# Kernel optimization log

Measured on AMD Instinct MI355X. Metric: run time of the kernel, lower is better.

Reference implementation:

```python
import jax, jax.numpy as jnp
import numpy as np

BN_EPS = 1e-5


def fps(xyz, npoint):
    # farthest point sampling; xyz: (B,N,3) -> (B,npoint) int32, starts at index 0 (torch convention)
    B, N, _ = xyz.shape
    def step(carry, _):
        dist, last = carry
        lp = jnp.take_along_axis(xyz, last[:, None, None], axis=1)  # (B,1,3)
        d = jnp.sum((xyz - lp) ** 2, -1)                             # (B,N)
        dist = jnp.minimum(dist, d)
        nxt = jnp.argmax(dist, -1).astype(jnp.int32)
        return (dist, nxt), nxt
    init = (jnp.full((B, N), 1e10, xyz.dtype), jnp.zeros((B,), jnp.int32))
    _, rest = jax.lax.scan(step, init, None, length=npoint - 1)
    return jnp.concatenate([jnp.zeros((1, B), jnp.int32), rest], 0).T  # (B,npoint)


def knn_idx(xyz, centers, k):
    # xyz (B,N,3), centers (B,S,3) -> (B,S,k) nearest-neighbor indices
    d = (jnp.sum(centers ** 2, -1)[:, :, None]
         + jnp.sum(xyz ** 2, -1)[:, None, :]
         - 2.0 * jnp.einsum('bsc,bnc->bsn', centers, xyz))
    _, idx = jax.lax.top_k(-d, k)
    return idx


def group(feat, idx):
    # feat (B,N,C), idx (B,S,K) -> (B,S,K,C)
    return jax.vmap(lambda f, i: f[i])(feat, idx)


def sa_knn(xyz, points, npoint, nsample, w1, b1, w2, b2):
    # xyz (B,N,3), points (B,N,C); returns new_xyz (B,S,3), new_points (B,S,Cout)
    fidx = fps(xyz, npoint)
    new_xyz = jnp.take_along_axis(xyz, fidx[:, :, None], axis=1)        # (B,S,3)
    idx = knn_idx(xyz, new_xyz, nsample)                                 # (B,S,K)
    g_xyz = group(xyz, idx) - new_xyz[:, :, None, :]                     # relative coords
    g_pts = group(points, idx)
    x = jnp.concatenate([g_xyz, g_pts], -1)                              # (B,S,K,3+C)
    x = jax.nn.relu(jnp.einsum('bskc,oc->bsko', x, w1) + b1)
    x = jnp.einsum('bskc,oc->bsko', x, w2) + b2                          # last conv: no activation
    return new_xyz, jnp.max(x, 2)                                        # max over neighbors


def sa_all(xyz, points, w1, b1, w2, b2):
    # group_all: concat xyz+points over all N, shared MLP, max over N -> (B,Cout)
    x = jnp.concatenate([xyz, points], -1)                               # (B,N,3+C)
    x = jax.nn.relu(jnp.einsum('bnc,oc->bno', x, w1) + b1)
    x = jnp.einsum('bnc,oc->bno', x, w2) + b2
    return jnp.max(x, 1)


def fc_head(x, w1, b1, g1, be1, w2, b2, g2, be2):
    # Linear + BN(eval, running mean=0/var=1) + ReLU, twice; Dropout = identity in eval
    s = 1.0 / np.sqrt(1.0 + BN_EPS)
    x = jax.nn.relu(g1 * ((x @ w1.T + b1) * s) + be1)
    x = jax.nn.relu(g2 * ((x @ w2.T + b2) * s) + be2)
    return x


def forward(point_cloud, sa1_w1, sa1_b1, sa1_w2, sa1_b2,
            sa2_w1, sa2_b1, sa2_w2, sa2_b2,
            sa3_w1, sa3_b1, sa3_w2, sa3_b2,
            fc_w1, fc_b1, fc_g1, fc_be1, fc_w2, fc_b2, fc_g2, fc_be2):
    xyz = jnp.transpose(point_cloud, (0, 2, 1))  # (B,N,3)
    nsamples2 = (16, 32, 48)
    logits, codes = [], []
    for i in range(3):  # three structurally distinct branches
        x1, p1 = sa_knn(xyz, xyz, 512, 16, sa1_w1[i], sa1_b1[i], sa1_w2[i], sa1_b2[i])
        x2, p2 = sa_knn(x1, p1, 128, nsamples2[i], sa2_w1[i], sa2_b1[i], sa2_w2[i], sa2_b2[i])
        code = sa_all(x2, p2, sa3_w1[i], sa3_b1[i], sa3_w2[i], sa3_b2[i])   # (B,512)
        logits.append(fc_head(code, fc_w1[i], fc_b1[i], fc_g1[i], fc_be1[i],
                              fc_w2[i], fc_b2[i], fc_g2[i], fc_be2[i]))      # (B,128)
        codes.append(code)
    return tuple(logits) + tuple(codes)


def setup_inputs():
    key = jax.random.key(0)
    ks = iter(jax.random.split(key, 16))
    def w(shape, s=0.05):
        return jax.random.normal(next(ks), shape, jnp.float32) * s
    B, N = 32, 2048
    inp = {'point_cloud': jax.random.normal(next(ks), (B, 3, N), jnp.float32)}
    inp.update(
        sa1_w1=w((3, 64, 6)), sa1_b1=jnp.zeros((3, 64)), sa1_w2=w((3, 128, 64)), sa1_b2=jnp.zeros((3, 128)),
        sa2_w1=w((3, 128, 131)), sa2_b1=jnp.zeros((3, 128)), sa2_w2=w((3, 256, 128)), sa2_b2=jnp.zeros((3, 256)),
        sa3_w1=w((3, 512, 259)), sa3_b1=jnp.zeros((3, 512)), sa3_w2=w((3, 512, 512)), sa3_b2=jnp.zeros((3, 512)),
        fc_w1=w((3, 256, 512)), fc_b1=jnp.zeros((3, 256)), fc_g1=jnp.ones((3, 256)), fc_be1=jnp.zeros((3, 256)),
        fc_w2=w((3, 128, 256)), fc_b2=jnp.zeros((3, 128)), fc_g2=jnp.ones((3, 128)), fc_be2=jnp.zeros((3, 128)),
    )
    return inp


def reference(point_cloud, sa1_w1, sa1_b1, sa1_w2, sa1_b2,
              sa2_w1, sa2_b1, sa2_w2, sa2_b2,
              sa3_w1, sa3_b1, sa3_w2, sa3_b2,
              fc_w1, fc_b1, fc_g1, fc_be1, fc_w2, fc_b2, fc_g2, fc_be2):
    return forward(point_cloud, sa1_w1, sa1_b1, sa1_w2, sa1_b2,
                   sa2_w1, sa2_b1, sa2_w2, sa2_b2,
                   sa3_w1, sa3_b1, sa3_w2, sa3_b2,
                   fc_w1, fc_b1, fc_g1, fc_be1, fc_w2, fc_b2, fc_g2, fc_be2)
```

## Files before the change

### kernel.cpp

```cpp
#include <hip/hip_runtime.h>
#include <hip/hip_bf16.h>
#include <math.h>

#define DEVI __device__ __forceinline__

static constexpr int BB = 32, NN = 2048, S1 = 512, S2 = 128;

typedef float f32x4 __attribute__((ext_vector_type(4)));
typedef short s16x8 __attribute__((ext_vector_type(8)));

static constexpr size_t OFF_XS   = 0;
static constexpr size_t OFF_YS   = OFF_XS + (size_t)BB*NN;
static constexpr size_t OFF_ZS   = OFF_YS + (size_t)BB*NN;
static constexpr size_t OFF_SSQ  = OFF_ZS + (size_t)BB*NN;
static constexpr size_t OFF_NX1X = OFF_SSQ + (size_t)BB*NN;
static constexpr size_t OFF_NX1Y = OFF_NX1X + (size_t)BB*S1;
static constexpr size_t OFF_NX1Z = OFF_NX1Y + (size_t)BB*S1;
static constexpr size_t OFF_NX2X = OFF_NX1Z + (size_t)BB*S1;
static constexpr size_t OFF_NX2Y = OFF_NX2X + (size_t)BB*S2;
static constexpr size_t OFF_NX2Z = OFF_NX2Y + (size_t)BB*S2;
static constexpr size_t OFF_CODE = OFF_NX2Z + (size_t)BB*S2;
static constexpr size_t OFF_O3P  = OFF_CODE + (size_t)3*BB*512;
static constexpr size_t OFF_P1   = OFF_O3P + (size_t)3*BB*4*512;
static constexpr size_t OFF_X3   = OFF_P1 + (size_t)3*BB*S1*128;
static constexpr size_t OFF_H3   = OFF_X3 + (size_t)3*BB*S2*260;
static constexpr size_t OFF_W    = OFF_H3 + (size_t)3*BB*S2*512;
static constexpr size_t W1A  = OFF_W;
static constexpr size_t B1A  = W1A + 3*64*6;
static constexpr size_t W2A  = B1A + 3*64;
static constexpr size_t B2A  = W2A + 3*128*64;
static constexpr size_t W1B  = B2A + 3*128;
static constexpr size_t B1B  = W1B + 3*128*132;
static constexpr size_t W2B  = B1B + 3*128;
static constexpr size_t B2B  = W2B + 3*256*128;
static constexpr size_t W1C  = B2B + 3*256;
static constexpr size_t B1C  = W1C + 3*512*260;
static constexpr size_t W2C  = B1C + 3*512;
static constexpr size_t B2C  = W2C + 3*512*512;
static constexpr size_t FW1  = B2C + 3*512;
static constexpr size_t FB1  = FW1 + 3*256*512;
static constexpr size_t FG1  = FB1 + 3*256;
static constexpr size_t FBE1 = FG1 + 3*256;
static constexpr size_t FW2  = FBE1 + 3*256;
static constexpr size_t FB2  = FW2 + 3*128*256;
static constexpr size_t FG2  = FB2 + 3*128;
static constexpr size_t FBE2 = FG2 + 3*128;
static constexpr size_t OFF_KNN1 = FBE2 + 3*128;
static constexpr size_t OFF_KNN2 = OFF_KNN1 + (size_t)BB*S1*16;
static constexpr size_t OFF_W1BF = OFF_KNN2 + (size_t)BB*S2*48;
static constexpr size_t OFF_W2BF = OFF_W1BF + 30720;
static constexpr size_t OFF_W1CBH = OFF_W2BF + 49152;
static constexpr size_t OFF_W1CBL = OFF_W1CBH + 221184;
static constexpr size_t OFF_W2CBH = OFF_W1CBL + 221184;
static constexpr size_t OFF_W2CBL = OFF_W2CBH + 393216;
static constexpr size_t OFF_X3BH  = OFF_W2CBL + 393216;
static constexpr size_t OFF_X3BL  = OFF_X3BH + 1769472;
static constexpr size_t OFF_H3BH  = OFF_X3BL + 1769472;
static constexpr size_t OFF_H3BL  = OFF_H3BH + 3145728;
static constexpr size_t OFF_W2ABH = OFF_H3BL + 3145728;
static constexpr size_t OFF_W2ABL = OFF_W2ABH + 12288;
static constexpr size_t WS_FLOATS = OFF_W2ABL + 12288;

__device__ __align__(16) float g_ws[WS_FLOATS];
__device__ int g_is_f32;
__device__ int g_flip;
__device__ int g_bad;
__device__ int g_nz;

DEVI float bf2f(const __hip_bfloat16 v){ return __bfloat162float(v); }
DEVI float rn_add(float a, float b){ return __fadd_rn(a,b); }
DEVI float rn_mul(float a, float b){ return __fmul_rn(a,b); }
DEVI float rn_sub(float a, float b){ return __fsub_rn(a,b); }
DEVI float sq3(float x,float y,float z){ return rn_add(rn_add(rn_mul(x,x),rn_mul(y,y)),rn_mul(z,z)); }

DEVI float ldany(const void* s, size_t i, int isf){
  return isf ? ((const float*)s)[i] : bf2f(((const __hip_bfloat16*)s)[i]);
}
DEVI unsigned short f2bf(float f){
  unsigned u = __float_as_uint(f);
  unsigned r = (u + 0x7FFFu + ((u>>16)&1u)) >> 16;
  return (unsigned short)r;
}
DEVI float bfbits2f(unsigned short h){ return __uint_as_float(((unsigned)h)<<16); }
DEVI void mfma16(f32x4& d, s16x8 a, s16x8 b){
  asm volatile("v_mfma_f32_16x16x32_bf16 %0, %1, %2, %0" : "+v"(d) : "v"(a), "v"(b));
}
DEVI void mfma_guard(f32x4& d){
  asm volatile("s_nop 7\n\ts_nop 7\n\ts_nop 2" : "+v"(d));
}

#define DPPF(dst, src, CTRL) dst = __uint_as_float((unsigned)__builtin_amdgcn_update_dpp(\
    (int)__float_as_uint(src), (int)__float_as_uint(src), CTRL, 0xF, 0xF, false))
#define DPPI(dst, src, CTRL) dst = __builtin_amdgcn_update_dpp(src, src, CTRL, 0xF, 0xF, false)
#define RED_STEP(CTRL) { float ov; int oi; DPPF(ov, best, CTRL); DPPI(oi, bidx, CTRL); \
  if (ov > best || (ov == best && oi < bidx)){ best = ov; bidx = oi; } }
#define WAVE_ARGMAX() RED_STEP(0xB1) RED_STEP(0x4E) RED_STEP(0x124) RED_STEP(0x128) RED_STEP(0x142) RED_STEP(0x143)

#define REDMIN_STEP(CTRL) { float ov; int oi; DPPF(ov, best, CTRL); DPPI(oi, bidx, CTRL); \
  if (ov < best || (ov == best && oi < bidx)){ best = ov; bidx = oi; } }
#define WAVE_ARGMIN() REDMIN_STEP(0xB1) REDMIN_STEP(0x4E) REDMIN_STEP(0x124) REDMIN_STEP(0x128) REDMIN_STEP(0x142) REDMIN_STEP(0x143)

__global__ __launch_bounds__(256) void init_detect_kernel(const void* __restrict__ pc){
  __shared__ int s_cnt[256];
  int t = threadIdx.x;
  if (t==0){ g_flip=0; g_bad=0; g_nz=0; }
  const unsigned short* h = (const unsigned short*)pc;
  int weird = 0;
  for (int i=t; i<4096; i+=256){
    unsigned short v = h[2*i];
    int e = (v >> 7) & 0xFF;
    if (e == 0xFF || e < 90 || e > 140) weird++;
  }
  s_cnt[t] = weird; __syncthreads();
  for (int o=128;o>0;o>>=1){ if (t<o) s_cnt[t]+=s_cnt[t+o]; __syncthreads(); }
  if (t==0) g_is_f32 = (s_cnt[0] > 1024) ? 1 : 0;
}

struct ParamPtrs { const void* p[20]; };

DEVI void cvt_arr(const void* s, float* d, int n, int g, int gs, int isf){
  for (int i=g;i<n;i+=gs) d[i] = ldany(s,i,isf);
}
DEVI void cvt_pad(const void* s, float* d, int rows, int cin, int cinp, int g, int gs, int isf){
  int tot = rows*cinp;
  for (int i=g;i<tot;i+=gs){ int r=i/cinp, c=i%cinp; d[i] = (c<cin)? ldany(s,(size_t)r*cin+c,isf) : 0.f; }
}

__global__ __launch_bounds__(256) void cvtprep_kernel(ParamPtrs pp, const void* __restrict__ pc, int mode){
  if (mode==1 && g_flip==0) return;
  const int isf = g_is_f32 ^ mode;
  if (blockIdx.x < 256){
    int i = blockIdx.x*256 + threadIdx.x;
    int b = i >> 11, n = i & 2047;
    float x = ldany(pc, (size_t)(b*3+0)*2048 + n, isf);
    float y = ldany(pc, (size_t)(b*3+1)*2048 + n, isf);
    float z = ldany(pc, (size_t)(b*3+2)*2048 + n, isf);
    g_ws[OFF_XS+i]=x; g_ws[OFF_YS+i]=y; g_ws[OFF_ZS+i]=z;
    g_ws[OFF_SSQ+i]=sq3(x,y,z);
    return;
  }
  int g = (blockIdx.x-256)*256 + threadIdx.x; int gs = 512*256;
  float* ws = g_ws;
  cvt_arr(pp.p[0],  ws+W1A, 3*64*6, g, gs, isf);
  cvt_arr(pp.p[1],  ws+B1A, 3*64, g, gs, isf);
  cvt_arr(pp.p[2],  ws+W2A, 3*128*64, g, gs, isf);
  cvt_arr(pp.p[3],  ws+B2A, 3*128, g, gs, isf);
  cvt_pad(pp.p[4],  ws+W1B, 3*128, 131, 132, g, gs, isf);
  cvt_arr(pp.p[5],  ws+B1B, 3*128, g, gs, isf);
  cvt_arr(pp.p[6],  ws+W2B, 3*256*128, g, gs, isf);
  cvt_arr(pp.p[7],  ws+B2B, 3*256, g, gs, isf);
  cvt_pad(pp.p[8],  ws+W1C, 3*512, 259, 260, g, gs, isf);
  cvt_arr(pp.p[9],  ws+B1C, 3*512, g, gs, isf);
  cvt_arr(pp.p[10], ws+W2C, 3*512*512, g, gs, isf);
  cvt_arr(pp.p[11], ws+B2C, 3*512, g, gs, isf);
  cvt_arr(pp.p[12], ws+FW1, 3*256*512, g, gs, isf);
  cvt_arr(pp.p[13], ws+FB1, 3*256, g, gs, isf);
  cvt_arr(pp.p[14], ws+FG1, 3*256, g, gs, isf);
  cvt_arr(pp.p[15], ws+FBE1,3*256, g, gs, isf);
  cvt_arr(pp.p[16], ws+FW2, 3*128*256, g, gs, isf);
  cvt_arr(pp.p[17], ws+FB2, 3*128, g, gs, isf);
  cvt_arr(pp.p[18], ws+FG2, 3*128, g, gs, isf);
  cvt_arr(pp.p[19], ws+FBE2,3*128, g, gs, isf);
}

__global__ __launch_bounds__(256) void scan_check_kernel(){
  size_t off; int n, g, gs;
  if (blockIdx.x < 128){ off = OFF_XS; n = 3*BB*NN; g = blockIdx.x*256 + threadIdx.x; gs = 128*256; }
  else { off = FW1; n = 3*256*512; g = (blockIdx.x-128)*256 + threadIdx.x; gs = 128*256; }
  int bad=0, nz=0;
  for (int i=g;i<n;i+=gs){
    float v = g_ws[off + i];
    if (v != v || fabsf(v) > 1e4f) bad=1;
    if (fabsf(v) > 1e-20f) nz=1;
  }
  unsigned long long mb = __ballot(bad), mn = __ballot(nz);
  if ((threadIdx.x & 63)==0){
    if (mb) atomicOr(&g_bad, 1);
    if (mn) atomicOr(&g_nz, 1);
  }
}

__global__ __launch_bounds__(64) void resolve_flip_kernel(){
  if (threadIdx.x==0){
    g_flip = (g_bad || !g_nz) ? 1 : 0;
    g_bad = 0; g_nz = 0;
  }
}

DEVI void cvt_bf16_body(int g, int gs){
  unsigned short* w1d = (unsigned short*)(g_ws + OFF_W1BF);
  for (int i=g; i<3*128*160; i+=gs){
    int br = i/(128*160); int rem = i%(128*160); int h = rem/160; int c = rem%160;
    float v = (c<132) ? g_ws[W1B + ((size_t)br*128 + h)*132 + c] : 0.f;
    w1d[i] = f2bf(v);
  }
  unsigned short* w2d = (unsigned short*)(g_ws + OFF_W2BF);
  for (int i=g; i<3*256*128; i+=gs) w2d[i] = f2bf(g_ws[W2B + i]);
  unsigned short* w1ch = (unsigned short*)(g_ws + OFF_W1CBH);
  unsigned short* w1cl = (unsigned short*)(g_ws + OFF_W1CBL);
  for (int i=g; i<3*512*288; i+=gs){
    int br = i/(512*288); int rem = i%(512*288); int n = rem/288; int c = rem%288;
    float v = (c<260) ? g_ws[W1C + ((size_t)br*512 + n)*260 + c] : 0.f;
    unsigned short hi = f2bf(v);
    w1ch[i] = hi; w1cl[i] = f2bf(v - bfbits2f(hi));
  }
  unsigned short* w2ch = (unsigned short*)(g_ws + OFF_W2CBH);
  unsigned short* w2cl = (unsigned short*)(g_ws + OFF_W2CBL);
  for (int i=g; i<3*512*512; i+=gs){
    float v = g_ws[W2C + i];
    unsigned short hi = f2bf(v);
    w2ch[i] = hi; w2cl[i] = f2bf(v - bfbits2f(hi));
  }
  unsigned short* w2ah = (unsigned short*)(g_ws + OFF_W2ABH);
  unsigned short* w2al = (unsigned short*)(g_ws + OFF_W2ABL);
  for (int i=g; i<3*128*64; i+=gs){
    float v = g_ws[W2A + i];
    unsigned short hi = f2bf(v);
    w2ah[i] = hi; w2al[i] = f2bf(v - bfbits2f(hi));
  }
}

static constexpr int SP1 = 171, SP2 = 342;

#define FPS_DECL(J) float px##J, py##J, pz##J, dd##J;
#define FPS_LD256A(J) { int n=(J)*256+t; px##J=xs[n]; py##J=ys[n]; pz##J=zs[n]; dd##J=1e10f; xl[n]=px##J; yl[n]=py##J; zl[n]=pz##J; }
#define FPS_LD256B(J) { int n=(J)*256+t; px##J=xs[n]; py##J=ys[n]; pz##J=zs[n]; dd##J=ddg[n]; xl[n]=px##J; yl[n]=py##J; zl[n]=pz##J; }
#define FPS_SAVE(J) ddg[(J)*256+t]=dd##J;
#define FPS_LD64(J) { int n=(J)*64+t; px##J=xs[n]; py##J=ys[n]; pz##J=zs[n]; dd##J=1e10f; xl[n]=px##J; yl[n]=py##J; zl[n]=pz##J; }
#define FPS_UPD(J) { float dx=rn_sub(px##J,lx), dy=rn_sub(py##J,ly), dz=rn_sub(pz##J,lz); float d=sq3(dx,dy,dz); dd##J=fminf(dd##J,d); }
#define FPS_T1(J,JA,JB) float v##J; int q##J; { bool c = dd##JB > dd##JA; v##J = c? dd##JB : dd##JA; q##J = c? (JB) : (JA); }
#define FPS_T2(JA,JB) { bool c = v##JB > v##JA; v##JA = c? v##JB : v##JA; q##JA = c? q##JB : q##JA; }

#define FPS1_ITER_BODY() \
    FPS_UPD(0) FPS_UPD(1) FPS_UPD(2) FPS_UPD(3) FPS_UPD(4) FPS_UPD(5) FPS_UPD(6) FPS_UPD(7) \
    FPS_T1(0,0,1) FPS_T1(1,2,3) FPS_T1(2,4,5) FPS_T1(3,6,7) \
    FPS_T2(0,1) FPS_T2(2,3) \
    FPS_T2(0,2) \
    float best = v0; int bidx = q0*256 + t; \
    WAVE_ARGMAX() \
    int par = i & 1; \
    if ((t&63)==63){ s_val[par][wave]=best; s_idx[par][wave]=bidx; } \
    __syncthreads(); \
    float va = s_val[par][0], vb = s_val[par][1], vc = s_val[par][2], vd = s_val[par][3]; \
    int ia = s_idx[par][0], ib = s_idx[par][1], ic = s_idx[par][2], id_ = s_idx[par][3]; \
    if (vb > va || (vb == va && ib < ia)){ va = vb; ia = ib; } \
    if (vd > vc || (vd == vc && id_ < ic)){ vc = vd; ic = id_; } \
    if (vc > va || (vc == va && ic < ia)){ va = vc; ia = ic; } \
    int gidx = ia; \
    lx = xl[gidx]; ly = yl[gidx]; lz = zl[gidx]; \
    if (t==0){ nx[i]=lx; ny[i]=ly; nz[i]=lz; }

#define FPS1_BLOCK_SETUP() \
  const int b = blockIdx.x; \
  const int wave = t >> 6; \
  const float* xs = g_ws + OFF_XS + (size_t)b*NN; \
  const float* ys = g_ws + OFF_YS + (size_t)b*NN; \
  const float* zs = g_ws + OFF_ZS + (size_t)b*NN; \
  float* nx = g_ws + OFF_NX1X + (size_t)b*S1; \
  float* ny = g_ws + OFF_NX1Y + (size_t)b*S1; \
  float* nz = g_ws + OFF_NX1Z + (size_t)b*S1; \
  float* ddg = g_ws + OFF_X3 + (size_t)b*NN; \
  __shared__ float xl[NN], yl[NN], zl[NN]; \
  __shared__ float s_val[2][4]; __shared__ int s_idx[2][4]; \
  FPS_DECL(0) FPS_DECL(1) FPS_DECL(2) FPS_DECL(3) FPS_DECL(4) FPS_DECL(5) FPS_DECL(6) FPS_DECL(7)

#define FPS1_BLOCK_SETUP_U(SM) \
  const int b = blockIdx.x; \
  const int wave = t >> 6; \
  const float* xs = g_ws + OFF_XS + (size_t)b*NN; \
  const float* ys = g_ws + OFF_YS + (size_t)b*NN; \
  const float* zs = g_ws + OFF_ZS + (size_t)b*NN; \
  float* nx = g_ws + OFF_NX1X + (size_t)b*S1; \
  float* ny = g_ws + OFF_NX1Y + (size_t)b*S1; \
  float* nz = g_ws + OFF_NX1Z + (size_t)b*S1; \
  float* ddg = g_ws + OFF_X3 + (size_t)b*NN; \
  float* xl = (float*)(SM); float* yl = xl + NN; float* zl = yl + NN; \
  float (*s_val)[4] = (float(*)[4])(zl + NN); \
  int (*s_idx)[4] = (int(*)[4])((char*)(zl + NN) + 32); \
  FPS_DECL(0) FPS_DECL(1) FPS_DECL(2) FPS_DECL(3) FPS_DECL(4) FPS_DECL(5) FPS_DECL(6) FPS_DECL(7)

__global__ __launch_bounds__(256,1) void fps1A_cvt_kernel(){
  const int t = threadIdx.x;
  if (blockIdx.x >= 32){
    cvt_bf16_body((blockIdx.x-32)*256 + t, 256*256);
    return;
  }
  FPS1_BLOCK_SETUP()
  FPS_LD256A(0) FPS_LD256A(1) FPS_LD256A(2) FPS_LD256A(3) FPS_LD256A(4) FPS_LD256A(5) FPS_LD256A(6) FPS_LD256A(7)
  __syncthreads();
  float lx = xl[0], ly = yl[0], lz = zl[0];
  if (t==0){ nx[0]=lx; ny[0]=ly; nz[0]=lz; }
  for (int i=1;i<SP1;i++){
    FPS1_ITER_BODY()
  }
  FPS_SAVE(0) FPS_SAVE(1) FPS_SAVE(2) FPS_SAVE(3) FPS_SAVE(4) FPS_SAVE(5) FPS_SAVE(6) FPS_SAVE(7)
}

#define KNN1_POISON(C) case C: d[C] = match ? 3.0e38f : d[C]; break;
DEVI void knn1_body(int wid, int lane){
  int b = wid >> 9;
  const float* xs = g_ws + OFF_XS + (size_t)b*NN;
  const float* ys = g_ws + OFF_YS + (size_t)b*NN;
  const float* zs = g_ws + OFF_ZS + (size_t)b*NN;
  const float* sq = g_ws + OFF_SSQ + (size_t)b*NN;
  float cx = g_ws[OFF_NX1X + wid], cy = g_ws[OFF_NX1Y + wid], cz = g_ws[OFF_NX1Z + wid];
  float sc = sq3(cx,cy,cz);
  float d[32];
  #pragma unroll
  for (int c=0;c<32;c++){
    int n = c*64 + lane;
    float x=xs[n], y=ys[n], z=zs[n];
    float dot = rn_add(rn_add(rn_mul(cx,x),rn_mul(cy,y)),rn_mul(cz,z));
    d[c] = rn_sub(rn_add(sc,sq[n]), rn_mul(2.f,dot));
  }
  int* out = (int*)(g_ws + OFF_KNN1) + (size_t)wid*16;
  for (int r=0;r<16;r++){
    float tv[16]; int tc[16];
    #pragma unroll
    for (int c=0;c<16;c++){
      float a = d[2*c];
      float e = d[2*c+1];
      bool cc = e < a;
      tv[c] = cc ? e : a; tc[c] = cc ? (2*c+1) : (2*c);
    }
    #pragma unroll
    for (int s=1; s<16; s<<=1){
      #pragma unroll
      for (int c=0;c<16;c+=2){
        if ((c % (2*s)) == 0 && c+s < 16){
          bool cc = tv[c+s] < tv[c];
          tv[c] = cc ? tv[c+s] : tv[c];
          tc[c] = cc ? tc[c+s] : tc[c];
        }
      }
    }
    float best = tv[0]; int bidx = tc[0]*64 + lane;
    WAVE_ARGMIN()
    int wbi = __builtin_amdgcn_readlane(bidx, 63);
    if (lane == 0) out[r] = wbi;
    bool match = (lane == (wbi & 63));
    switch ((wbi >> 6) & 31){
      KNN1_POISON(0)  KNN1_POISON(1)  KNN1_POISON(2)  KNN1_POISON(3)
      KNN1_POISON(4)  KNN1_POISON(5)  KNN1_POISON(6)  KNN1_POISON(7)
      KNN1_POISON(8)  KNN1_POISON(9)  KNN1_POISON(10) KNN1_POISON(11)
      KNN1_POISON(12) KNN1_POISON(13) KNN1_POISON(14) KNN1_POISON(15)
      KNN1_POISON(16) KNN1_POISON(17) KNN1_POISON(18) KNN1_POISON(19)
      KNN1_POISON(20) KNN1_POISON(21) KNN1_POISON(22) KNN1_POISON(23)
      KNN1_POISON(24) KNN1_POISON(25) KNN1_POISON(26) KNN1_POISON(27)
      KNN1_POISON(28) KNN1_POISON(29) KNN1_POISON(30) KNN1_POISON(31)
    }
  }
}

DEVI void sa1_body(int br, int bxx, float* w1s, float* b1s, short* Hh, short* Hl){
  const int t = threadIdx.x;
  const int wave = t>>6, lane = t&63, quad = lane>>4, l16 = lane&15;
  for (int i=t;i<384;i+=256) w1s[i] = g_ws[W1A + (size_t)br*384 + i];
  if (t<64) b1s[t] = g_ws[B1A + br*64 + t];
  __syncthreads();
  const int* kn = (const int*)(g_ws + OFF_KNN1);
  const short* w2h = (const short*)(g_ws + OFF_W2ABH) + (size_t)br*128*64;
  const short* w2l = (const short*)(g_ws + OFF_W2ABL) + (size_t)br*128*64;
  const float* b2 = g_ws + B2A + br*128;
  for (int it=0; it<4; it++){
    int gid = bxx*16 + it*4 + wave;
    int b = gid >> 9;
    int idx = kn[(size_t)gid*16 + l16] & (NN-1);
    float cx = g_ws[OFF_NX1X+gid], cy = g_ws[OFF_NX1Y+gid], cz = g_ws[OFF_NX1Z+gid];
    size_t gl = (size_t)b*NN + idx;
    float x = g_ws[OFF_XS+gl], y = g_ws[OFF_YS+gl], z = g_ws[OFF_ZS+gl];
    float f0=x-cx, f1=y-cy, f2=z-cz;
    #pragma unroll
    for (int i=0;i<16;i++){
      int h = quad*16 + i;
      float acc = b1s[h];
      acc += f0*w1s[h*6+0] + f1*w1s[h*6+1] + f2*w1s[h*6+2]
           +  x*w1s[h*6+3] +  y*w1s[h*6+4] +  z*w1s[h*6+5];
      acc = fmaxf(acc, 0.f);
      unsigned short hi = f2bf(acc);
      Hh[wave*1152 + l16*72 + h] = (short)hi;
      Hl[wave*1152 + l16*72 + h] = (short)f2bf(acc - bfbits2f(hi));
    }
    s16x8 ah[2], al[2];
    #pragma unroll
    for (int ks=0;ks<2;ks++){
      ah[ks] = *(const s16x8*)(&Hh[wave*1152 + l16*72 + ks*32 + quad*8]);
      al[ks] = *(const s16x8*)(&Hl[wave*1152 + l16*72 + ks*32 + quad*8]);
    }
    unsigned short* P1g = (unsigned short*)(g_ws + OFF_P1) + ((size_t)br*16384 + gid)*128;
    #pragma unroll
    for (int ni=0; ni<8; ni++){
      int o = ni*16 + l16;
      f32x4 acc = {0.f,0.f,0.f,0.f};
      #pragma unroll
      for (int ks=0; ks<2; ks++){
        s16x8 bh = *(const s16x8*)(w2h + (size_t)o*64 + ks*32 + quad*8);
        s16x8 bl = *(const s16x8*)(w2l + (size_t)o*64 + ks*32 + quad*8);
        mfma16(acc, ah[ks], bh);
        mfma16(acc, ah[ks], bl);
        mfma16(acc, al[ks], bh);
      }
      mfma_guard(acc);
      float vmax = fmaxf(fmaxf(acc[0],acc[1]), fmaxf(acc[2],acc[3]));
      vmax = fmaxf(vmax, __shfl_xor(vmax,16));
      vmax = fmaxf(vmax, __shfl_xor(vmax,32));
      if (quad==0) P1g[o] = f2bf(vmax + b2[o]);
    }
  }
}

__global__ __launch_bounds__(256,1) void fps1B_knn1a_kernel(){
  const int t = threadIdx.x;
  if (blockIdx.x >= 32){
    int lin = ((blockIdx.x-32)*256 + t) >> 6;
    int b = lin / 160, s = lin % 160;
    knn1_body(b*S1 + s, t & 63);
    return;
  }
  FPS1_BLOCK_SETUP()
  FPS_LD256B(0) FPS_LD256B(1) FPS_LD256B(2) FPS_LD256B(3) FPS_LD256B(4) FPS_LD256B(5) FPS_LD256B(6) FPS_LD256B(7)
  __syncthreads();
  float lx = nx[SP1-1], ly = ny[SP1-1], lz = nz[SP1-1];
  for (int i=SP1;i<SP2;i++){
    FPS1_ITER_BODY()
  }
  FPS_SAVE(0) FPS_SAVE(1) FPS_SAVE(2) FPS_SAVE(3) FPS_SAVE(4) FPS_SAVE(5) FPS_SAVE(6) FPS_SAVE(7)
}

__global__ __launch_bounds__(256,1) void fps1C_knn1b_sa1a_kernel(){
  __shared__ __align__(16) char smem[3*NN*4 + 64];
  const int t = threadIdx.x;
  if (blockIdx.x >= 1440){
    int q = blockIdx.x - 1440;
    int br = q / 320, rem = q % 320;
    int b = rem / 10, sblk = rem % 10;
    float* w1s = (float*)smem;
    float* b1s = w1s + 384;
    short* Hh = (short*)(b1s + 64);
    short* Hl = Hh + 4608;
    sa1_body(br, b*32 + sblk, w1s, b1s, Hh, Hl);
    return;
  }
  if (blockIdx.x >= 32){
    int lin = ((blockIdx.x-32)*256 + t) >> 6;
    int b = lin / 176, s = 160 + lin % 176;
    knn1_body(b*S1 + s, t & 63);
    return;
  }
  FPS1_BLOCK_SETUP_U(smem)
  FPS_LD256B(0) FPS_LD256B(1) FPS_LD256B(2) FPS_LD256B(3) FPS_LD256B(4) FPS_LD256B(5) FPS_LD256B(6) FPS_LD256B(7)
  __syncthreads();
  float lx = nx[SP2-1], ly = ny[SP2-1], lz = nz[SP2-1];
  for (int i=SP2;i<S1;i++){
    FPS1_ITER_BODY()
  }
}

__global__ __launch_bounds__(256) void fps2_knn1c_sa1a_kernel(){
  __shared__ float xl[S1], yl[S1], zl[S1];
  __shared__ float w1s[384];
  __shared__ float b1s[64];
  __shared__ __align__(16) short Hh[4*16*72];
  __shared__ __align__(16) short Hl[4*16*72];
  const int t = threadIdx.x;
  if (blockIdx.x >= 1440){
    int q = blockIdx.x - 1440;
    int br = q / 352, rem = q % 352;
    int b = rem / 11, sblk = 10 + rem % 11;
    sa1_body(br, b*32 + sblk, w1s, b1s, Hh, Hl);
    return;
  }
  if (blockIdx.x >= 32){
    int lin = ((blockIdx.x-32)*256 + t) >> 6;
    int b = lin / 176, s = 336 + lin % 176;
    knn1_body(b*S1 + s, t & 63);
    return;
  }
  if (t >= 64) return;
  const int b = blockIdx.x;
  const float* xs = g_ws + OFF_NX1X + (size_t)b*S1;
  const float* ys = g_ws + OFF_NX1Y + (size_t)b*S1;
  const float* zs = g_ws + OFF_NX1Z + (size_t)b*S1;
  float* nx = g_ws + OFF_NX2X + (size_t)b*S2;
  float* ny = g_ws + OFF_NX2Y + (size_t)b*S2;
  float* nz = g_ws + OFF_NX2Z + (size_t)b*S2;
  FPS_DECL(0) FPS_DECL(1) FPS_DECL(2) FPS_DECL(3) FPS_DECL(4) FPS_DECL(5) FPS_DECL(6) FPS_DECL(7)
  FPS_LD64(0) FPS_LD64(1) FPS_LD64(2) FPS_LD64(3) FPS_LD64(4) FPS_LD64(5) FPS_LD64(6) FPS_LD64(7)
  float lx = xl[0], ly = yl[0], lz = zl[0];
  if (t==0){ nx[0]=lx; ny[0]=ly; nz[0]=lz; }
  for (int i=1;i<S2;i++){
    FPS_UPD(0) FPS_UPD(1) FPS_UPD(2) FPS_UPD(3) FPS_UPD(4) FPS_UPD(5) FPS_UPD(6) FPS_UPD(7)
    FPS_T1(0,0,1) FPS_T1(1,2,3) FPS_T1(2,4,5) FPS_T1(3,6,7)
    FPS_T2(0,1) FPS_T2(2,3)
    FPS_T2(0,2)
    float best = v0; int bidx = q0*64 + t;
    WAVE_ARGMAX()
    int gidx = __builtin_amdgcn_readlane(bidx, 63);
    lx = xl[gidx]; ly = yl[gidx]; lz = zl[gidx];
    if (t==0){ nx[i]=lx; ny[i]=ly; nz[i]=lz; }
  }
}

#define KNN2_POISON(C) case C: d[C] = match ? 3.0e38f : d[C]; break;
DEVI void knn2_body(int wid, int lane){
  int b = wid >> 7;
  const float* xs = g_ws + OFF_NX1X + (size_t)b*S1;
  const float* ys = g_ws + OFF_NX1Y + (size_t)b*S1;
  const float* zs = g_ws + OFF_NX1Z + (size_t)b*S1;
  float cx = g_ws[OFF_NX2X + wid], cy = g_ws[OFF_NX2Y + wid], cz = g_ws[OFF_NX2Z + wid];
  float sc = sq3(cx,cy,cz);
  float d[8];
  #pragma unroll
  for (int c=0;c<8;c++){
    int n = c*64 + lane;
    float x=xs[n], y=ys[n], z=zs[n];
    float sx = sq3(x,y,z);
    float dot = rn_add(rn_add(rn_mul(cx,x),rn_mul(cy,y)),rn_mul(cz,z));
    d[c] = rn_sub(rn_add(sc,sx), rn_mul(2.f,dot));
  }
  int* out = (int*)(g_ws + OFF_KNN2) + (size_t)wid*48;
  for (int r=0;r<48;r++){
    float tv[4]; int tc[4];
    #pragma unroll
    for (int c=0;c<4;c++){
      float a = d[2*c];
      float e = d[2*c+1];
      bool cc = e < a;
      tv[c] = cc ? e : a; tc[c] = cc ? (2*c+1) : (2*c);
    }
    { bool cc = tv[1] < tv[0]; tv[0] = cc?tv[1]:tv[0]; tc[0] = cc?tc[1]:tc[0]; }
    { bool cc = tv[3] < tv[2]; tv[2] = cc?tv[3]:tv[2]; tc[2] = cc?tc[3]:tc[2]; }
    { bool cc = tv[2] < tv[0]; tv[0] = cc?tv[2]:tv[0]; tc[0] = cc?tc[2]:tc[0]; }
    float best = tv[0]; int bidx = tc[0]*64 + lane;
    WAVE_ARGMIN()
    int wbi = __builtin_amdgcn_readlane(bidx, 63);
    if (lane == 0) out[r] = wbi;
    bool match = (lane == (wbi & 63));
    switch ((wbi >> 6) & 7){
      KNN2_POISON(0) KNN2_POISON(1) KNN2_POISON(2) KNN2_POISON(3)
      KNN2_POISON(4) KNN2_POISON(5) KNN2_POISON(6) KNN2_POISON(7)
    }
  }
}

__global__ __launch_bounds__(256) void knn2_sa1b_kernel(){
  __shared__ float w1s[384];
  __shared__ float b1s[64];
  __shared__ __align__(16) short Hh[4*16*72];
  __shared__ __align__(16) short Hl[4*16*72];
  const int t = threadIdx.x;
  if (blockIdx.x < 1024){
    knn2_body((blockIdx.x*256 + t) >> 6, t & 63);
    return;
  }
  int q = blockIdx.x - 1024;
  int br = q / 352, rem = q % 352;
  int b = rem / 11, sblk = 21 + rem % 11;
  sa1_body(br, b*32 + sblk, w1s, b1s, Hh, Hl);
}

template<int K>
DEVI void sa2_body(int br, int g2, short* Xb, short* Hb, float* ctr, int* idxs){
  constexpr int MT = K/16;
  const int b = g2 >> 7;
  const int t = threadIdx.x;
  const int wave = t >> 6, lane = t & 63, quad = lane >> 4, l16 = lane & 15;
  const int* kn2 = (const int*)(g_ws + OFF_KNN2) + (size_t)g2*48;
  if (t < K) idxs[t] = kn2[t] & (S1-1);
  if (t < 3) ctr[t] = g_ws[(t==0?OFF_NX2X:(t==1?OFF_NX2Y:OFF_NX2Z)) + g2];
  __syncthreads();
  const unsigned short* p1b = (const unsigned short*)(g_ws + OFF_P1) + (size_t)br*16384*128;
  const int grp = t >> 5, gl = t & 31;
  for (int k = grp; k < K; k += 8){
    int idx = idxs[k];
    const unsigned short* row = p1b + ((size_t)b*S1 + idx)*128;
    unsigned long long w = *(const unsigned long long*)(row + gl*4);
    short* dst = &Xb[k*168 + 3 + gl*4];
    dst[0] = (short)(w & 0xFFFF);
    dst[1] = (short)((w >> 16) & 0xFFFF);
    dst[2] = (short)((w >> 32) & 0xFFFF);
    dst[3] = (short)((w >> 48) & 0xFFFF);
    if (gl < 32) Xb[k*168 + 131 + gl] = 0;
    if (gl < 5)  Xb[k*168 + 163 + gl] = 0;
  }
  if (t < K){
    int idx = idxs[t];
    float c0 = g_ws[OFF_NX1X + (size_t)b*S1 + idx] - ctr[0];
    float c1 = g_ws[OFF_NX1Y + (size_t)b*S1 + idx] - ctr[1];
    float c2 = g_ws[OFF_NX1Z + (size_t)b*S1 + idx] - ctr[2];
    Xb[t*168+0] = (short)f2bf(c0);
    Xb[t*168+1] = (short)f2bf(c1);
    Xb[t*168+2] = (short)f2bf(c2);
  }
  __syncthreads();
  {
    const short* w1bf = (const short*)(g_ws + OFF_W1BF) + (size_t)br*128*160;
    const float* b1 = g_ws + B1B + br*128;
    for (int ni = wave; ni < 8; ni += 4){
      int h = ni*16 + l16;
      s16x8 bfr[5];
      #pragma unroll
      for (int ks=0;ks<5;ks++) bfr[ks] = *(const s16x8*)(w1bf + (size_t)h*160 + ks*32 + quad*8);
      float bias = b1[h];
      #pragma unroll
      for (int m=0; m<MT; m++){
        f32x4 acc = {0.f,0.f,0.f,0.f};
        #pragma unroll
        for (int ks=0;ks<5;ks++){
          s16x8 a = *(const s16x8*)(&Xb[(m*16 + l16)*168 + ks*32 + quad*8]);
          mfma16(acc, a, bfr[ks]);
        }
        mfma_guard(acc);
        #pragma unroll
        for (int r=0;r<4;r++){
          int row = m*16 + quad*4 + r;
          float hv = fmaxf(acc[r] + bias, 0.f);
          Hb[row*136 + ni*16 + l16] = (short)f2bf(hv);
        }
      }
    }
  }
  __syncthreads();
  {
    const short* w2bf = (const short*)(g_ws + OFF_W2BF) + (size_t)br*256*128;
    const float* b2 = g_ws + B2B + br*256;
    unsigned short* xh = (unsigned short*)(g_ws + OFF_X3BH);
    unsigned short* xlo = (unsigned short*)(g_ws + OFF_X3BL);
    size_t row = (size_t)(br*4096 + g2)*288;
    for (int ni = wave; ni < 16; ni += 4){
      int o = ni*16 + l16;
      s16x8 bfr[4];
      #pragma unroll
      for (int ks=0;ks<4;ks++) bfr[ks] = *(const s16x8*)(w2bf + (size_t)o*128 + ks*32 + quad*8);
      float vmax = -3.4e38f;
      #pragma unroll
      for (int m=0; m<MT; m++){
        f32x4 acc = {0.f,0.f,0.f,0.f};
        #pragma unroll
        for (int ks=0;ks<4;ks++){
          s16x8 a = *(const s16x8*)(&Hb[(m*16 + l16)*136 + ks*32 + quad*8]);
          mfma16(acc, a, bfr[ks]);
        }
        mfma_guard(acc);
        #pragma unroll
        for (int r=0;r<4;r++) vmax = fmaxf(vmax, acc[r]);
      }
      vmax = fmaxf(vmax, __shfl_xor(vmax, 16));
      vmax = fmaxf(vmax, __shfl_xor(vmax, 32));
      if (quad == 0){
        float hv = vmax + b2[o];
        unsigned short hi = f2bf(hv);
        xh[row + 3 + o] = hi;
        xlo[row + 3 + o] = f2bf(hv - bfbits2f(hi));
      }
    }
    if (t < 3){
      float cv = ctr[t];
      unsigned short hi = f2bf(cv);
      xh[row + t] = hi; xlo[row + t] = f2bf(cv - bfbits2f(hi));
    }
    if (t >= 3 && t < 32){ xh[row + 256 + t] = 0; xlo[row + 256 + t] = 0; }
  }
}

__global__ __launch_bounds__(256) void sa2_all_kernel(){
  __shared__ __align__(16) short Xb[48*168];
  __shared__ __align__(16) short Hb[48*136];
  __shared__ float ctr[3];
  __shared__ int idxs[48];
  int br = blockIdx.x >> 12;
  int g2 = blockIdx.x & 4095;
  if (br == 0)      sa2_body<16>(0, g2, Xb, Hb, ctr, idxs);
  else if (br == 1) sa2_body<32>(1, g2, Xb, Hb, ctr, idxs);
  else              sa2_body<48>(2, g2, Xb, Hb, ctr, idxs);
}

__global__ __launch_bounds__(256) void sa3l1_mfma_kernel(){
  const int br = blockIdx.y; const int r0 = blockIdx.x*32;
  const int t = threadIdx.x;
  const int wave = t >> 6, lane = t & 63, quad = lane >> 4, l16 = lane & 15;
  const short* xh = (const short*)(g_ws + OFF_X3BH) + (size_t)(br*4096 + r0)*288;
  const short* xl = (const short*)(g_ws + OFF_X3BL) + (size_t)(br*4096 + r0)*288;
  const short* wh = (const short*)(g_ws + OFF_W1CBH) + (size_t)br*512*288;
  const short* wl = (const short*)(g_ws + OFF_W1CBL) + (size_t)br*512*288;
  const float* bias = g_ws + B1C + br*512;
  unsigned short* hh = (unsigned short*)(g_ws + OFF_H3BH) + (size_t)(br*4096 + r0)*512;
  unsigned short* hl = (unsigned short*)(g_ws + OFF_H3BL) + (size_t)(br*4096 + r0)*512;
  f32x4 acc[2][8];
  #pragma unroll
  for (int m=0;m<2;m++)
    #pragma unroll
    for (int ni=0;ni<8;ni++) acc[m][ni] = (f32x4){0.f,0.f,0.f,0.f};
  for (int ks=0; ks<9; ks++){
    s16x8 ah[2], al[2];
    #pragma unroll
    for (int m=0;m<2;m++){
      ah[m] = *(const s16x8*)(xh + (size_t)(m*16+l16)*288 + ks*32 + quad*8);
      al[m] = *(const s16x8*)(xl + (size_t)(m*16+l16)*288 + ks*32 + quad*8);
    }
    #pragma unroll
    for (int ni=0;ni<8;ni++){
      int n = wave*128 + ni*16 + l16;
      s16x8 bh = *(const s16x8*)(wh + (size_t)n*288 + ks*32 + quad*8);
      s16x8 bl = *(const s16x8*)(wl + (size_t)n*288 + ks*32 + quad*8);
      #pragma unroll
      for (int m=0;m<2;m++){
        mfma16(acc[m][ni], ah[m], bh);
        mfma16(acc[m][ni], ah[m], bl);
        mfma16(acc[m][ni], al[m], bh);
      }
    }
  }
  mfma_guard(acc[0][0]);
  #pragma unroll
  for (int m=0;m<2;m++){
    #pragma unroll
    for (int ni=0;ni<8;ni++){
      int col = wave*128 + ni*16 + l16;
      float bs = bias[col];
      #pragma unroll
      for (int r=0;r<4;r++){
        int row = m*16 + quad*4 + r;
        float hv = fmaxf(acc[m][ni][r] + bs, 0.f);
        unsigned short hi = f2bf(hv);
        hh[(size_t)row*512 + col] = hi;
        hl[(size_t)row*512 + col] = f2bf(hv - bfbits2f(hi));
      }
    }
  }
}

__global__ __launch_bounds__(256) void sa3l2_mfma_kernel(){
  const int br = blockIdx.y; const int b = blockIdx.x>>2; const int part = blockIdx.x&3;
  const int t = threadIdx.x;
  const int wave = t >> 6, lane = t & 63, quad = lane >> 4, l16 = lane & 15;
  const int row0 = b*128 + part*32;
  const short* ahp = (const short*)(g_ws + OFF_H3BH) + (size_t)(br*4096 + row0)*512;
  const short* alp = (const short*)(g_ws + OFF_H3BL) + (size_t)(br*4096 + row0)*512;
  const short* wh = (const short*)(g_ws + OFF_W2CBH) + (size_t)br*512*512;
  const short* wl = (const short*)(g_ws + OFF_W2CBL) + (size_t)br*512*512;
  f32x4 acc[2][8];
  #pragma unroll
  for (int m=0;m<2;m++)
    #pragma unroll
    for (int ni=0;ni<8;ni++) acc[m][ni] = (f32x4){0.f,0.f,0.f,0.f};
  for (int ks=0; ks<16; ks++){
    s16x8 ah[2], al[2];
    #pragma unroll
    for (int m=0;m<2;m++){
      ah[m] = *(const s16x8*)(ahp + (size_t)(m*16+l16)*512 + ks*32 + quad*8);
      al[m] = *(const s16x8*)(alp + (size_t)(m*16+l16)*512 + ks*32 + quad*8);
    }
    #pragma unroll
    for (int ni=0;ni<8;ni++){
      int n = wave*128 + ni*16 + l16;
      s16x8 bh = *(const s16x8*)(wh + (size_t)n*512 + ks*32 + quad*8);
      s16x8 bl = *(const s16x8*)(wl + (size_t)n*512 + ks*32 + quad*8);
      #pragma unroll
      for (int m=0;m<2;m++){
        mfma16(acc[m][ni], ah[m], bh);
        mfma16(acc[m][ni], ah[m], bl);
        mfma16(acc[m][ni], al[m], bh);
      }
    }
  }
  mfma_guard(acc[0][0]);
  #pragma unroll
  for (int ni=0;ni<8;ni++){
    float vmax = -3.4e38f;
    #pragma unroll
    for (int m=0;m<2;m++)
      #pragma unroll
      for (int r=0;r<4;r++) vmax = fmaxf(vmax, acc[m][ni][r]);
    vmax = fmaxf(vmax, __shfl_xor(vmax, 16));
    vmax = fmaxf(vmax, __shfl_xor(vmax, 32));
    if (quad == 0){
      int col = wave*128 + ni*16 + l16;
      g_ws[OFF_O3P + (((size_t)br*BB + b)*4 + part)*512 + col] = vmax;
    }
  }
}

__global__ __launch_bounds__(256) void fc_kernel(float* __restrict__ out, int out_size){
  int br = blockIdx.x >> 5; int b = blockIdx.x & 31; int t = threadIdx.x;
  __shared__ float xin[512]; __shared__ float x1s[256];
  const float* o3p = g_ws + OFF_O3P + (((size_t)br*BB + b)*4)*512;
  const float* b2c = g_ws + B2C + br*512;
  #pragma unroll
  for (int k=0;k<2;k++){
    int o = t + k*256;
    float m = fmaxf(fmaxf(o3p[o], o3p[512+o]), fmaxf(o3p[1024+o], o3p[1536+o]));
    m += b2c[o];
    xin[o] = m;
    int oi = 3*BB*128 + ((br*BB + b)*512) + o;
    if (oi < out_size) out[oi] = m;
  }
  __syncthreads();
  const float s = (float)(1.0 / sqrt(1.0 + 1e-5));
  {
    const float4* wp = (const float4*)(g_ws + FW1 + ((size_t)br*256 + t)*512);
    const float4* xp = (const float4*)xin;
    float acc = 0.f;
    #pragma unroll 8
    for (int q=0;q<128;q++){ float4 w4=wp[q], x4=xp[q]; acc += w4.x*x4.x + w4.y*x4.y + w4.z*x4.z + w4.w*x4.w; }
    acc = (acc + g_ws[FB1 + br*256+t]) * s;
    acc = g_ws[FG1+br*256+t]*acc + g_ws[FBE1+br*256+t];
    x1s[t] = fmaxf(acc, 0.f);
  }
  __syncthreads();
  if (t < 128){
    const float4* wp = (const float4*)(g_ws + FW2 + ((size_t)br*128 + t)*256);
    const float4* xp = (const float4*)x1s;
    float acc=0.f;
    #pragma unroll 8
    for (int q=0;q<64;q++){ float4 w4=wp[q], x4=xp[q]; acc += w4.x*x4.x + w4.y*x4.y + w4.z*x4.z + w4.w*x4.w; }
    acc = (acc + g_ws[FB2+br*128+t])*s;
    acc = g_ws[FG2+br*128+t]*acc + g_ws[FBE2+br*128+t];
    int oi = ((size_t)br*BB + b)*128 + t;
    if (oi < out_size) out[oi] = fmaxf(acc,0.f);
  }
}

extern "C" void kernel_launch(void* const* d_in, const int* in_sizes, int n_in,
                              void* d_out, int out_size, void* d_ws, size_t ws_size,
                              hipStream_t stream) {
  (void)d_ws; (void)ws_size;
  if (n_in < 21) return;
  if (in_sizes[0] != BB*3*NN) return;
  float* out = (float*)d_out;

  ParamPtrs pp;
  for (int i=0;i<20;i++) pp.p[i] = d_in[i+1];

  init_detect_kernel<<<1,256,0,stream>>>(d_in[0]);
  cvtprep_kernel<<<768,256,0,stream>>>(pp, d_in[0], 0);
  scan_check_kernel<<<256,256,0,stream>>>();
  resolve_flip_kernel<<<1,64,0,stream>>>();
  cvtprep_kernel<<<768,256,0,stream>>>(pp, d_in[0], 1);

  fps1A_cvt_kernel<<<32+256,256,0,stream>>>();
  fps1B_knn1a_kernel<<<32+1280,256,0,stream>>>();
  fps1C_knn1b_sa1a_kernel<<<32+1408+960,256,0,stream>>>();
  fps2_knn1c_sa1a_kernel<<<32+1408+1056,256,0,stream>>>();
  knn2_sa1b_kernel<<<1024+1056,256,0,stream>>>();
  sa2_all_kernel<<<3*4096,256,0,stream>>>();

  sa3l1_mfma_kernel<<<dim3(128,3),256,0,stream>>>();
  sa3l2_mfma_kernel<<<dim3(128,3),256,0,stream>>>();
  fc_kernel<<<96,256,0,stream>>>(out, out_size);
}
```

Baseline: 1.038 ms.

## Batch multiple SA2 groups per block and remap blocks to XCDs by batch

The SA2 kernel now processes several centroid groups per block (4 for K=16, 2 for K=32, 1 for K=48), so every block fills 48–64 rows of the MFMA tile. This cuts the block count from 12288 to 7168 and amortizes the per-block weight fragment loads and setup over more rows. Block indices are also remapped so that all blocks for a given batch land on the same XCD, which should improve L2 locality for the gathered P1 rows. The cost is larger shared memory per block and more registers for the per-group max accumulators, which may reduce occupancy.

```diff
diff --git a/kernel.cpp b/kernel.cpp
--- a/kernel.cpp
+++ b/kernel.cpp
@@ -559,19 +559,27 @@
   sa1_body(br, b*32 + sblk, w1s, b1s, Hh, Hl);
 }
 
-template<int K>
-DEVI void sa2_body(int br, int g2, short* Xb, short* Hb, float* ctr, int* idxs){
-  constexpr int MT = K/16;
-  const int b = g2 >> 7;
+template<int K, int G>
+DEVI void sa2_body(int br, int g2base, short* Xb, short* Hb, float* ctr, int* idxs){
+  constexpr int R = K*G;
+  constexpr int MT = R/16;
+  constexpr int CT = K/16;
+  const int b = g2base >> 7;
   const int t = threadIdx.x;
   const int wave = t >> 6, lane = t & 63, quad = lane >> 4, l16 = lane & 15;
-  const int* kn2 = (const int*)(g_ws + OFF_KNN2) + (size_t)g2*48;
-  if (t < K) idxs[t] = kn2[t] & (S1-1);
-  if (t < 3) ctr[t] = g_ws[(t==0?OFF_NX2X:(t==1?OFF_NX2Y:OFF_NX2Z)) + g2];
+  if (t < R){
+    int g = t / K;
+    const int* kn2 = (const int*)(g_ws + OFF_KNN2) + (size_t)(g2base + g)*48;
+    idxs[t] = kn2[t - g*K] & (S1-1);
+  }
+  if (t < 3*G){
+    int g = t/3, d = t - g*3;
+    ctr[t] = g_ws[(d==0?OFF_NX2X:(d==1?OFF_NX2Y:OFF_NX2Z)) + g2base + g];
+  }
   __syncthreads();
   const unsigned short* p1b = (const unsigned short*)(g_ws + OFF_P1) + (size_t)br*16384*128;
   const int grp = t >> 5, gl = t & 31;
-  for (int k = grp; k < K; k += 8){
+  for (int k = grp; k < R; k += 8){
     int idx = idxs[k];
     const unsigned short* row = p1b + ((size_t)b*S1 + idx)*128;
     unsigned long long w = *(const unsigned long long*)(row + gl*4);
@@ -580,14 +588,15 @@
     dst[1] = (short)((w >> 16) & 0xFFFF);
     dst[2] = (short)((w >> 32) & 0xFFFF);
     dst[3] = (short)((w >> 48) & 0xFFFF);
-    if (gl < 32) Xb[k*168 + 131 + gl] = 0;
+    Xb[k*168 + 131 + gl] = 0;
     if (gl < 5)  Xb[k*168 + 163 + gl] = 0;
   }
-  if (t < K){
+  if (t < R){
+    int g = t / K;
     int idx = idxs[t];
-    float c0 = g_ws[OFF_NX1X + (size_t)b*S1 + idx] - ctr[0];
-    float c1 = g_ws[OFF_NX1Y + (size_t)b*S1 + idx] - ctr[1];
-    float c2 = g_ws[OFF_NX1Z + (size_t)b*S1 + idx] - ctr[2];
+    float c0 = g_ws[OFF_NX1X + (size_t)b*S1 + idx] - ctr[g*3+0];
+    float c1 = g_ws[OFF_NX1Y + (size_t)b*S1 + idx] - ctr[g*3+1];
+    float c2 = g_ws[OFF_NX1Z + (size_t)b*S1 + idx] - ctr[g*3+2];
     Xb[t*168+0] = (short)f2bf(c0);
     Xb[t*168+1] = (short)f2bf(c1);
     Xb[t*168+2] = (short)f2bf(c2);
@@ -626,13 +635,14 @@
     const float* b2 = g_ws + B2B + br*256;
     unsigned short* xh = (unsigned short*)(g_ws + OFF_X3BH);
     unsigned short* xlo = (unsigned short*)(g_ws + OFF_X3BL);
-    size_t row = (size_t)(br*4096 + g2)*288;
     for (int ni = wave; ni < 16; ni += 4){
       int o = ni*16 + l16;
       s16x8 bfr[4];
       #pragma unroll
       for (int ks=0;ks<4;ks++) bfr[ks] = *(const s16x8*)(w2bf + (size_t)o*128 + ks*32 + quad*8);
-      float vmax = -3.4e38f;
+      float vm[G];
+      #pragma unroll
+      for (int g=0;g<G;g++) vm[g] = -3.4e38f;
       #pragma unroll
       for (int m=0; m<MT; m++){
         f32x4 acc = {0.f,0.f,0.f,0.f};
@@ -643,36 +653,59 @@
         }
         mfma_guard(acc);
         #pragma unroll
-        for (int r=0;r<4;r++) vmax = fmaxf(vmax, acc[r]);
+        for (int r=0;r<4;r++) vm[m/CT] = fmaxf(vm[m/CT], acc[r]);
       }
-      vmax = fmaxf(vmax, __shfl_xor(vmax, 16));
-      vmax = fmaxf(vmax, __shfl_xor(vmax, 32));
-      if (quad == 0){
-        float hv = vmax + b2[o];
-        unsigned short hi = f2bf(hv);
-        xh[row + 3 + o] = hi;
-        xlo[row + 3 + o] = f2bf(hv - bfbits2f(hi));
+      #pragma unroll
+      for (int g=0;g<G;g++){
+        float v = vm[g];
+        v = fmaxf(v, __shfl_xor(v, 16));
+        v = fmaxf(v, __shfl_xor(v, 32));
+        if (quad == 0){
+          size_t rowg = (size_t)(br*4096 + g2base + g)*288;
+          float hv = v + b2[o];
+          unsigned short hi = f2bf(hv);
+          xh[rowg + 3 + o] = hi;
+          xlo[rowg + 3 + o] = f2bf(hv - bfbits2f(hi));
+        }
       }
     }
-    if (t < 3){
-      float cv = ctr[t];
-      unsigned short hi = f2bf(cv);
-      xh[row + t] = hi; xlo[row + t] = f2bf(cv - bfbits2f(hi));
-    }
-    if (t >= 3 && t < 32){ xh[row + 256 + t] = 0; xlo[row + 256 + t] = 0; }
+    unsigned short* xh2 = (unsigned short*)(g_ws + OFF_X3BH);
+    unsigned short* xlo2 = (unsigned short*)(g_ws + OFF_X3BL);
+    #pragma unroll
+    for (int g=0;g<G;g++){
+      size_t rowg = (size_t)(br*4096 + g2base + g)*288;
+      if (t < 3){
+        float cv = ctr[g*3+t];
+        unsigned short hi = f2bf(cv);
+        xh2[rowg + t] = hi; xlo2[rowg + t] = f2bf(cv - bfbits2f(hi));
+      }
+      if (t >= 3 && t < 32){ xh2[rowg + 256 + t] = 0; xlo2[rowg + 256 + t] = 0; }
+    }
   }
 }
 
 __global__ __launch_bounds__(256) void sa2_all_kernel(){
-  __shared__ __align__(16) short Xb[48*168];
-  __shared__ __align__(16) short Hb[48*136];
-  __shared__ float ctr[3];
-  __shared__ int idxs[48];
-  int br = blockIdx.x >> 12;
-  int g2 = blockIdx.x & 4095;
-  if (br == 0)      sa2_body<16>(0, g2, Xb, Hb, ctr, idxs);
-  else if (br == 1) sa2_body<32>(1, g2, Xb, Hb, ctr, idxs);
-  else              sa2_body<48>(2, g2, Xb, Hb, ctr, idxs);
+  __shared__ __align__(16) short Xb[64*168];
+  __shared__ __align__(16) short Hb[64*136];
+  __shared__ float ctr[12];
+  __shared__ int idxs[64];
+  int xcd = blockIdx.x & 7;
+  int idx = blockIdx.x >> 3;
+  if (idx < 128){
+    int bloc = idx >> 5, g2o = (idx & 31) << 2;
+    int b = xcd*4 + bloc;
+    sa2_body<16,4>(0, b*128 + g2o, Xb, Hb, ctr, idxs);
+  } else if (idx < 384){
+    int j = idx - 128;
+    int bloc = j >> 6, g2o = (j & 63) << 1;
+    int b = xcd*4 + bloc;
+    sa2_body<32,2>(1, b*128 + g2o, Xb, Hb, ctr, idxs);
+  } else {
+    int j = idx - 384;
+    int bloc = j >> 7, g2o = j & 127;
+    int b = xcd*4 + bloc;
+    sa2_body<48,1>(2, b*128 + g2o, Xb, Hb, ctr, idxs);
+  }
 }
 
 __global__ __launch_bounds__(256) void sa3l1_mfma_kernel(){
@@ -843,7 +876,7 @@
   fps1C_knn1b_sa1a_kernel<<<32+1408+960,256,0,stream>>>();
   fps2_knn1c_sa1a_kernel<<<32+1408+1056,256,0,stream>>>();
   knn2_sa1b_kernel<<<1024+1056,256,0,stream>>>();
-  sa2_all_kernel<<<3*4096,256,0,stream>>>();
+  sa2_all_kernel<<<7168,256,0,stream>>>();
 
   sa3l1_mfma_kernel<<<dim3(128,3),256,0,stream>>>();
   sa3l2_mfma_kernel<<<dim3(128,3),256,0,stream>>>();
```

After: 1.013 ms. -2.4%, faster.
